# Performance work log

Measured on AMD Instinct MI355X. Metric: run time of the kernel, lower is better.

## Reference

```python
import jax, jax.numpy as jnp
import numpy as np

# ---- static configuration (matches init_kwargs / input_specs) ----
B, N = 4, 128            # images, proposals per image
C = 256                  # feature channels (in_channels)
HF, WF = 23, 30          # feature map size (input 736x960 / 32)
PH, PW = 7, 7            # pooled_size
SCALE = 1.0 / 32.0       # scale_factor
HIMG, WIMG = HF * 32, WF * 32
KH = HF // PH + 2        # max rows any pooling bin can span
KW = WF // PW + 2        # max cols any pooling bin can span
HID, OUT = 256, 5
NEG = -1e30


def _roi_pool_one(f, box):
    """Quantized ROI max pooling for one proposal.
    f: (C, HF, WF) feature map; box: (4,) [x1,y1,x2,y2] in feature coords.
    Returns (C, PH, PW)."""
    box = jax.lax.stop_gradient(box)  # indices are non-differentiable
    x1 = jnp.clip(jnp.floor(box[0]).astype(jnp.int32), 0, WF - 1)
    y1 = jnp.clip(jnp.floor(box[1]).astype(jnp.int32), 0, HF - 1)
    roi_w = jnp.clip(jnp.ceil(box[2]).astype(jnp.int32) - x1, 1, WF)
    roi_h = jnp.clip(jnp.ceil(box[3]).astype(jnp.int32) - y1, 1, HF)
    ph = jnp.arange(PH)
    pw = jnp.arange(PW)
    hs = y1 + (ph * roi_h) // PH                       # bin row starts (PH,)
    he = y1 + ((ph + 1) * roi_h + PH - 1) // PH        # bin row ends (ceil)
    ws = x1 + (pw * roi_w) // PW
    we = x1 + ((pw + 1) * roi_w + PW - 1) // PW
    hidx = hs[:, None] + jnp.arange(KH)[None, :]       # (PH, KH)
    hval = (hidx < he[:, None]) & (hidx < HF)
    widx = ws[:, None] + jnp.arange(KW)[None, :]       # (PW, KW)
    wval = (widx < we[:, None]) & (widx < WF)
    rows = f[:, jnp.clip(hidx, 0, HF - 1), :]          # (C, PH, KH, WF) gather
    rmax = jnp.max(jnp.where(hval[None, :, :, None], rows, NEG), axis=2)  # (C, PH, WF)
    cols = rmax[:, :, jnp.clip(widx, 0, WF - 1)]       # (C, PH, PW, KW) gather
    return jnp.max(jnp.where(wval[None, None], cols, NEG), axis=3)        # (C, PH, PW)


# vmap over proposals, then over images: (B,C,HF,WF),(B,N,4) -> (B,N,C,PH,PW)
_roi_pool = jax.vmap(jax.vmap(_roi_pool_one, in_axes=(None, 0)), in_axes=(0, 0))


def setup_inputs() -> dict:
    key = jax.random.key(0)
    ks = jax.random.split(key, 8)
    features = jax.random.normal(ks[0], (B, C, HF, WF), jnp.float32)
    # valid proposals in image coordinates (min box side ~32 px)
    x1 = jax.random.uniform(ks[1], (B, N)) * (WIMG - 32.0)
    y1 = jax.random.uniform(ks[2], (B, N)) * (HIMG - 32.0)
    x2 = x1 + 32.0 + jax.random.uniform(ks[3], (B, N)) * (WIMG - 32.0 - x1)
    y2 = y1 + 32.0 + jax.random.uniform(ks[4], (B, N)) * (HIMG - 32.0 - y1)
    conf = jax.random.normal(ks[5], (B, N))
    proposals = jnp.stack([x1, y1, x2, y2, conf], axis=-1)  # (B, N, 5)
    W1 = jax.random.normal(ks[6], (HID, C * PH * PW), jnp.float32) * 0.01
    b1 = jnp.zeros((HID,), jnp.float32)
    W2 = jax.random.normal(ks[7], (OUT, HID), jnp.float32) * 0.01
    b2 = jnp.zeros((OUT,), jnp.float32)
    return {"features": features, "proposals": proposals,
            "W1": W1, "b1": b1, "W2": W2, "b2": b2}


def reference(features, proposals, W1, b1, W2, b2):
    boxes_feat = proposals[..., :4] * SCALE                 # image -> feature coords
    pooled = _roi_pool(features, boxes_feat)                # (B, N, C, PH, PW)
    flat = pooled.reshape(B, N, C * PH * PW)
    h = jax.nn.relu(jnp.einsum('bnf,hf->bnh', flat, W1) + b1)
    out = jnp.einsum('bnh,oh->bno', h, W2) + b2             # (B, N, 5)
    refined_boxes = proposals[..., :4] + out[..., :4]
    refined_conf = jax.nn.sigmoid(proposals[..., 4:5] + out[..., 4:5])
    return jnp.concatenate([refined_boxes, refined_conf], axis=-1)  # (B, N, 5)
```

## Files before the change

### kernel.cpp

```cpp
#include <hip/hip_runtime.h>
#include <math.h>

#define Bq 4
#define Nq 128
#define Cq 256
#define HFq 23
#define WFq 30
#define PHq 7
#define PWq 7
#define HIDq 256
#define OUTq 5
#define Fq (Cq*PHq*PWq)
#define Mq (Bq*Nq)
#define HWq (HFq*WFq)
#define SCALEq (1.0f/32.0f)
#define NEGq (-1e30f)
#define KHq 5
#define KWq 6
#define SPLITK 14
#define KCH (Fq/SPLITK)
#define KSTEPS (KCH/32)

typedef float f32x4 __attribute__((ext_vector_type(4)));
typedef __bf16 bf16x8 __attribute__((ext_vector_type(8)));

__device__ __forceinline__ unsigned short f2b(float f) {
    unsigned int u = __float_as_uint(f);
    unsigned int r = (u + 0x7FFFu + ((u >> 16) & 1u)) >> 16;
    return (unsigned short)r;
}

__global__ __launch_bounds__(256) void k_transpose(const float* __restrict__ feat,
                                                   float* __restrict__ ft) {
    __shared__ float t[32][33];
    int bb = blockIdx.z;
    const float* src = feat + (size_t)bb * Cq * HWq;
    float* dst = ft + (size_t)bb * HWq * Cq;
    int x0 = blockIdx.x * 32;
    int c0 = blockIdx.y * 32;
    int tx = threadIdx.x, ty = threadIdx.y;
#pragma unroll
    for (int i = 0; i < 4; ++i) {
        int c = c0 + ty + i * 8;
        int x = x0 + tx;
        if (x < HWq) t[ty + i * 8][tx] = src[(size_t)c * HWq + x];
    }
    __syncthreads();
#pragma unroll
    for (int i = 0; i < 4; ++i) {
        int x = x0 + ty + i * 8;
        int c = c0 + tx;
        if (x < HWq) dst[(size_t)x * Cq + c] = t[tx][ty + i * 8];
    }
}

__global__ __launch_bounds__(256) void k_w1perm(const float* __restrict__ W1,
                                                unsigned short* __restrict__ w1p) {
    __shared__ __align__(16) unsigned short s[Fq];
    int j = blockIdx.x;
    const float4* src = (const float4*)(W1 + (size_t)j * Fq);
    for (int i = threadIdx.x; i < Fq / 4; i += 256) {
        float4 v = src[i];
        ushort4 o;
        o.x = f2b(v.x); o.y = f2b(v.y); o.z = f2b(v.z); o.w = f2b(v.w);
        ((ushort4*)s)[i] = o;
    }
    __syncthreads();
    uint4* dst = (uint4*)(w1p + (size_t)j * Fq);
    for (int i = threadIdx.x; i < Fq / 8; i += 256) {
        int base = i * 8;
        int cell = base >> 8;
        int c0 = base & 255;
        unsigned short tmp[8];
#pragma unroll
        for (int u = 0; u < 8; ++u) tmp[u] = s[(c0 + u) * 49 + cell];
        dst[i] = *(const uint4*)tmp;
    }
}

__global__ __launch_bounds__(256) void k_pool(const float* __restrict__ ft,
                                              const float* __restrict__ props,
                                              unsigned short* __restrict__ pooled) {
    int wave = threadIdx.x >> 6;
    int lane = threadIdx.x & 63;
    int g = blockIdx.y * 4 + wave;
    int m = blockIdx.x;
    int b = m >> 7;
    const float* pr = props + (size_t)m * 5;
    float b0 = pr[0] * SCALEq, b1v = pr[1] * SCALEq;
    float b2v = pr[2] * SCALEq, b3v = pr[3] * SCALEq;
    int x1 = min(max((int)floorf(b0), 0), WFq - 1);
    int y1 = min(max((int)floorf(b1v), 0), HFq - 1);
    int rw = min(max((int)ceilf(b2v) - x1, 1), WFq);
    int rh = min(max((int)ceilf(b3v) - y1, 1), HFq);
    const float* ftb = ft + (size_t)b * HWq * Cq + lane * 4;
    unsigned short* pm = pooled + (size_t)m * Fq + lane * 4;

    for (int cell = g; cell < PHq * PWq; cell += 8) {
        int ph = cell / 7;
        int pw = cell - ph * 7;
        int hs = y1 + (ph * rh) / PHq;
        int he = min(y1 + ((ph + 1) * rh + PHq - 1) / PHq, HFq);
        int ws = x1 + (pw * rw) / PWq;
        int we = min(x1 + ((pw + 1) * rw + PWq - 1) / PWq, WFq);
        f32x4 acc = {NEGq, NEGq, NEGq, NEGq};
#pragma unroll
        for (int kh = 0; kh < KHq; ++kh) {
            if (hs + kh < he) {
                const float* rowp = ftb + (size_t)((hs + kh) * WFq) * Cq;
#pragma unroll
                for (int kw = 0; kw < KWq; ++kw) {
                    if (ws + kw < we) {
                        f32x4 v = *(const f32x4*)(rowp + (size_t)(ws + kw) * Cq);
                        acc.x = fmaxf(acc.x, v.x);
                        acc.y = fmaxf(acc.y, v.y);
                        acc.z = fmaxf(acc.z, v.z);
                        acc.w = fmaxf(acc.w, v.w);
                    }
                }
            }
        }
        ushort4 o;
        o.x = f2b(acc.x); o.y = f2b(acc.y); o.z = f2b(acc.z); o.w = f2b(acc.w);
        *(ushort4*)(pm + (size_t)cell * Cq) = o;
    }
}

__global__ __launch_bounds__(256) void k_gemm1(const unsigned short* __restrict__ pooled,
                                               const unsigned short* __restrict__ w1p,
                                               float* __restrict__ part) {
    __shared__ __align__(16) unsigned short As[64 * 32];
    __shared__ __align__(16) unsigned short Bs[64 * 32];
    int m0 = blockIdx.x * 64;
    int j0 = blockIdx.y * 64;
    int kz = blockIdx.z;
    int tid = threadIdx.x;
    int r = tid >> 2, qq = tid & 3;
    const uint4* ap = (const uint4*)(pooled + (size_t)(m0 + r) * Fq + (size_t)kz * KCH + qq * 8);
    const uint4* bp = (const uint4*)(w1p + (size_t)(j0 + r) * Fq + (size_t)kz * KCH + qq * 8);
    int lane = tid & 63, wv = tid >> 6;
    int q = lane >> 4, mr = lane & 15;
    f32x4 acc0 = {0.f, 0.f, 0.f, 0.f};
    f32x4 acc1 = {0.f, 0.f, 0.f, 0.f};
    f32x4 acc2 = {0.f, 0.f, 0.f, 0.f};
    f32x4 acc3 = {0.f, 0.f, 0.f, 0.f};
    const bf16x8* afp = (const bf16x8*)(As + (wv * 16 + mr) * 32 + q * 8);
    const bf16x8* bfp0 = (const bf16x8*)(Bs + (0 + mr) * 32 + q * 8);
    const bf16x8* bfp1 = (const bf16x8*)(Bs + (16 + mr) * 32 + q * 8);
    const bf16x8* bfp2 = (const bf16x8*)(Bs + (32 + mr) * 32 + q * 8);
    const bf16x8* bfp3 = (const bf16x8*)(Bs + (48 + mr) * 32 + q * 8);
    uint4* asw = (uint4*)(As + r * 32 + qq * 8);
    uint4* bsw = (uint4*)(Bs + r * 32 + qq * 8);
    uint4 av = ap[0];
    uint4 bv = bp[0];
    for (int s = 0; s < KSTEPS; ++s) {
        __syncthreads();
        *asw = av;
        *bsw = bv;
        __syncthreads();
        if (s + 1 < KSTEPS) {
            av = ap[(s + 1) * 4];
            bv = bp[(s + 1) * 4];
        }
        bf16x8 a = *afp;
        acc0 = __builtin_amdgcn_mfma_f32_16x16x32_bf16(a, *bfp0, acc0, 0, 0, 0);
        acc1 = __builtin_amdgcn_mfma_f32_16x16x32_bf16(a, *bfp1, acc1, 0, 0, 0);
        acc2 = __builtin_amdgcn_mfma_f32_16x16x32_bf16(a, *bfp2, acc2, 0, 0, 0);
        acc3 = __builtin_amdgcn_mfma_f32_16x16x32_bf16(a, *bfp3, acc3, 0, 0, 0);
    }
    float* pbase = part + (size_t)kz * Mq * HIDq;
    int mb = m0 + wv * 16 + q * 4;
    int jj = j0 + mr;
#pragma unroll
    for (int r2 = 0; r2 < 4; ++r2) {
        float* row = pbase + (size_t)(mb + r2) * HIDq + jj;
        row[0]  = acc0[r2];
        row[16] = acc1[r2];
        row[32] = acc2[r2];
        row[48] = acc3[r2];
    }
}

__global__ __launch_bounds__(256) void k_reduce(const float* __restrict__ part,
                                                const float* __restrict__ b1,
                                                float* __restrict__ h) {
    int m = blockIdx.x, j = threadIdx.x;
    float s = 0.f;
#pragma unroll
    for (int z = 0; z < SPLITK; ++z) s += part[((size_t)z * Mq + m) * HIDq + j];
    s += b1[j];
    h[(size_t)m * HIDq + j] = fmaxf(s, 0.f);
}

__global__ __launch_bounds__(256) void k_final(const float* __restrict__ h,
                                               const float* __restrict__ W2,
                                               const float* __restrict__ b2,
                                               const float* __restrict__ props,
                                               float* __restrict__ out) {
    __shared__ float red[OUTq][4];
    int m = blockIdx.x, j = threadIdx.x;
    float hv = h[(size_t)m * HIDq + j];
    float p[OUTq];
#pragma unroll
    for (int o = 0; o < OUTq; ++o) p[o] = hv * W2[(size_t)o * HIDq + j];
    int lane = j & 63, wid = j >> 6;
#pragma unroll
    for (int o = 0; o < OUTq; ++o) {
        float v = p[o];
        v += __shfl_xor(v, 1);
        v += __shfl_xor(v, 2);
        v += __shfl_xor(v, 4);
        v += __shfl_xor(v, 8);
        v += __shfl_xor(v, 16);
        v += __shfl_xor(v, 32);
        if (lane == 0) red[o][wid] = v;
    }
    __syncthreads();
    if (j < OUTq) {
        float s = red[j][0] + red[j][1] + red[j][2] + red[j][3] + b2[j];
        float pv = props[(size_t)m * 5 + j];
        float r;
        if (j < 4) r = pv + s;
        else r = 1.f / (1.f + expf(-(pv + s)));
        out[(size_t)m * 5 + j] = r;
    }
}

extern "C" void kernel_launch(void* const* d_in, const int* in_sizes, int n_in,
                              void* d_out, int out_size, void* d_ws, size_t ws_size,
                              hipStream_t stream) {
    const float* feat  = (const float*)d_in[0];
    const float* props = (const float*)d_in[1];
    const float* W1    = (const float*)d_in[2];
    const float* b1    = (const float*)d_in[3];
    const float* W2    = (const float*)d_in[4];
    const float* b2    = (const float*)d_in[5];
    float* out = (float*)d_out;

    char* ws = (char*)d_ws;
    float* ft              = (float*)(ws);
    unsigned short* w1p    = (unsigned short*)(ws + 2826240);
    unsigned short* pooled = (unsigned short*)(ws + 9248768);
    float* part            = (float*)(ws + 22093824);
    float* h               = (float*)(ws + 29433856);

    k_transpose<<<dim3(22, 8, 4), dim3(32, 8), 0, stream>>>(feat, ft);
    k_w1perm<<<HIDq, 256, 0, stream>>>(W1, w1p);
    k_pool<<<dim3(Mq, 2), 256, 0, stream>>>(ft, props, pooled);
    k_gemm1<<<dim3(8, 4, SPLITK), 256, 0, stream>>>(pooled, w1p, part);
    k_reduce<<<Mq, 256, 0, stream>>>(part, b1, h);
    k_final<<<Mq, 256, 0, stream>>>(h, W2, b2, props, out);
}
```

Measured before the change: 128.7 us.

## Merge prep and tail kernels, store features as bf16, double-buffer GEMM LDS

After: 131.2 us. About the same (+2.0%).

```diff
diff --git a/kernel.cpp b/kernel.cpp
--- a/kernel.cpp
+++ b/kernel.cpp
@@ -17,9 +17,10 @@
 #define NEGq (-1e30f)
 #define KHq 5
 #define KWq 6
-#define SPLITK 14
+#define SPLITK 8
 #define KCH (Fq/SPLITK)
 #define KSTEPS (KCH/32)
+#define TJOBS 704
 
 typedef float f32x4 __attribute__((ext_vector_type(4)));
 typedef __bf16 bf16x8 __attribute__((ext_vector_type(8)));
@@ -29,56 +30,65 @@
     unsigned int r = (u + 0x7FFFu + ((u >> 16) & 1u)) >> 16;
     return (unsigned short)r;
 }
-
-__global__ __launch_bounds__(256) void k_transpose(const float* __restrict__ feat,
-                                                   float* __restrict__ ft) {
-    __shared__ float t[32][33];
-    int bb = blockIdx.z;
-    const float* src = feat + (size_t)bb * Cq * HWq;
-    float* dst = ft + (size_t)bb * HWq * Cq;
-    int x0 = blockIdx.x * 32;
-    int c0 = blockIdx.y * 32;
-    int tx = threadIdx.x, ty = threadIdx.y;
-#pragma unroll
-    for (int i = 0; i < 4; ++i) {
-        int c = c0 + ty + i * 8;
-        int x = x0 + tx;
-        if (x < HWq) t[ty + i * 8][tx] = src[(size_t)c * HWq + x];
-    }
-    __syncthreads();
-#pragma unroll
-    for (int i = 0; i < 4; ++i) {
-        int x = x0 + ty + i * 8;
-        int c = c0 + tx;
-        if (x < HWq) dst[(size_t)x * Cq + c] = t[tx][ty + i * 8];
-    }
-}
-
-__global__ __launch_bounds__(256) void k_w1perm(const float* __restrict__ W1,
-                                                unsigned short* __restrict__ w1p) {
-    __shared__ __align__(16) unsigned short s[Fq];
-    int j = blockIdx.x;
-    const float4* src = (const float4*)(W1 + (size_t)j * Fq);
-    for (int i = threadIdx.x; i < Fq / 4; i += 256) {
-        float4 v = src[i];
-        ushort4 o;
-        o.x = f2b(v.x); o.y = f2b(v.y); o.z = f2b(v.z); o.w = f2b(v.w);
-        ((ushort4*)s)[i] = o;
-    }
-    __syncthreads();
-    uint4* dst = (uint4*)(w1p + (size_t)j * Fq);
-    for (int i = threadIdx.x; i < Fq / 8; i += 256) {
-        int base = i * 8;
-        int cell = base >> 8;
-        int c0 = base & 255;
-        unsigned short tmp[8];
-#pragma unroll
-        for (int u = 0; u < 8; ++u) tmp[u] = s[(c0 + u) * 49 + cell];
-        dst[i] = *(const uint4*)tmp;
-    }
-}
-
-__global__ __launch_bounds__(256) void k_pool(const float* __restrict__ ft,
+__device__ __forceinline__ float b2f(unsigned short s) {
+    return __uint_as_float(((unsigned int)s) << 16);
+}
+
+union PrepSM {
+    float t[32][33];
+    unsigned short s[Fq];
+};
+
+__global__ __launch_bounds__(256) void k_prep(const float* __restrict__ feat,
+                                              const float* __restrict__ W1,
+                                              unsigned short* __restrict__ ft,
+                                              unsigned short* __restrict__ w1p) {
+    __shared__ __align__(16) PrepSM sm;
+    int tid = threadIdx.x, bid = blockIdx.x;
+    if (bid < TJOBS) {
+        int bb = bid / 176;
+        int rem = bid - bb * 176;
+        int cblk = rem / 22;
+        int xblk = rem - cblk * 22;
+        const float* src = feat + (size_t)bb * Cq * HWq;
+        unsigned short* dst = ft + (size_t)bb * HWq * Cq;
+        int x0 = xblk * 32, c0 = cblk * 32;
+        int tx = tid & 31, ty = tid >> 5;
+#pragma unroll
+        for (int i = 0; i < 4; ++i) {
+            int c = c0 + ty + i * 8, x = x0 + tx;
+            if (x < HWq) sm.t[ty + i * 8][tx] = src[(size_t)c * HWq + x];
+        }
+        __syncthreads();
+#pragma unroll
+        for (int i = 0; i < 4; ++i) {
+            int x = x0 + ty + i * 8, c = c0 + tx;
+            if (x < HWq) dst[(size_t)x * Cq + c] = f2b(sm.t[tx][ty + i * 8]);
+        }
+    } else {
+        int j = bid - TJOBS;
+        const float4* src = (const float4*)(W1 + (size_t)j * Fq);
+        for (int i = tid; i < Fq / 4; i += 256) {
+            float4 v = src[i];
+            ushort4 o;
+            o.x = f2b(v.x); o.y = f2b(v.y); o.z = f2b(v.z); o.w = f2b(v.w);
+            ((ushort4*)sm.s)[i] = o;
+        }
+        __syncthreads();
+        uint4* dst = (uint4*)(w1p + (size_t)j * Fq);
+        for (int i = tid; i < Fq / 8; i += 256) {
+            int base = i * 8;
+            int cell = base >> 8;
+            int c0 = base & 255;
+            unsigned short tmp[8];
+#pragma unroll
+            for (int u = 0; u < 8; ++u) tmp[u] = sm.s[(c0 + u) * 49 + cell];
+            dst[i] = *(const uint4*)tmp;
+        }
+    }
+}
+
+__global__ __launch_bounds__(256) void k_pool(const unsigned short* __restrict__ ft,
                                               const float* __restrict__ props,
                                               unsigned short* __restrict__ pooled) {
     int wave = threadIdx.x >> 6;
@@ -93,7 +103,7 @@
     int y1 = min(max((int)floorf(b1v), 0), HFq - 1);
     int rw = min(max((int)ceilf(b2v) - x1, 1), WFq);
     int rh = min(max((int)ceilf(b3v) - y1, 1), HFq);
-    const float* ftb = ft + (size_t)b * HWq * Cq + lane * 4;
+    const unsigned short* ftb = ft + (size_t)b * HWq * Cq + lane * 4;
     unsigned short* pm = pooled + (size_t)m * Fq + lane * 4;
 
     for (int cell = g; cell < PHq * PWq; cell += 8) {
@@ -101,21 +111,21 @@
         int pw = cell - ph * 7;
         int hs = y1 + (ph * rh) / PHq;
         int he = min(y1 + ((ph + 1) * rh + PHq - 1) / PHq, HFq);
-        int ws = x1 + (pw * rw) / PWq;
-        int we = min(x1 + ((pw + 1) * rw + PWq - 1) / PWq, WFq);
+        int wss = x1 + (pw * rw) / PWq;
+        int wee = min(x1 + ((pw + 1) * rw + PWq - 1) / PWq, WFq);
         f32x4 acc = {NEGq, NEGq, NEGq, NEGq};
 #pragma unroll
         for (int kh = 0; kh < KHq; ++kh) {
             if (hs + kh < he) {
-                const float* rowp = ftb + (size_t)((hs + kh) * WFq) * Cq;
+                const unsigned short* rowp = ftb + (size_t)((hs + kh) * WFq) * Cq;
 #pragma unroll
                 for (int kw = 0; kw < KWq; ++kw) {
-                    if (ws + kw < we) {
-                        f32x4 v = *(const f32x4*)(rowp + (size_t)(ws + kw) * Cq);
-                        acc.x = fmaxf(acc.x, v.x);
-                        acc.y = fmaxf(acc.y, v.y);
-                        acc.z = fmaxf(acc.z, v.z);
-                        acc.w = fmaxf(acc.w, v.w);
+                    if (wss + kw < wee) {
+                        ushort4 v = *(const ushort4*)(rowp + (size_t)(wss + kw) * Cq);
+                        acc.x = fmaxf(acc.x, b2f(v.x));
+                        acc.y = fmaxf(acc.y, b2f(v.y));
+                        acc.z = fmaxf(acc.z, b2f(v.z));
+                        acc.w = fmaxf(acc.w, b2f(v.w));
                     }
                 }
             }
@@ -129,8 +139,8 @@
 __global__ __launch_bounds__(256) void k_gemm1(const unsigned short* __restrict__ pooled,
                                                const unsigned short* __restrict__ w1p,
                                                float* __restrict__ part) {
-    __shared__ __align__(16) unsigned short As[64 * 32];
-    __shared__ __align__(16) unsigned short Bs[64 * 32];
+    __shared__ __align__(16) unsigned short As[2][2048];
+    __shared__ __align__(16) unsigned short Bs[2][2048];
     int m0 = blockIdx.x * 64;
     int j0 = blockIdx.y * 64;
     int kz = blockIdx.z;
@@ -144,29 +154,24 @@
     f32x4 acc1 = {0.f, 0.f, 0.f, 0.f};
     f32x4 acc2 = {0.f, 0.f, 0.f, 0.f};
     f32x4 acc3 = {0.f, 0.f, 0.f, 0.f};
-    const bf16x8* afp = (const bf16x8*)(As + (wv * 16 + mr) * 32 + q * 8);
-    const bf16x8* bfp0 = (const bf16x8*)(Bs + (0 + mr) * 32 + q * 8);
-    const bf16x8* bfp1 = (const bf16x8*)(Bs + (16 + mr) * 32 + q * 8);
-    const bf16x8* bfp2 = (const bf16x8*)(Bs + (32 + mr) * 32 + q * 8);
-    const bf16x8* bfp3 = (const bf16x8*)(Bs + (48 + mr) * 32 + q * 8);
-    uint4* asw = (uint4*)(As + r * 32 + qq * 8);
-    uint4* bsw = (uint4*)(Bs + r * 32 + qq * 8);
     uint4 av = ap[0];
     uint4 bv = bp[0];
     for (int s = 0; s < KSTEPS; ++s) {
-        __syncthreads();
-        *asw = av;
-        *bsw = bv;
+        int p = s & 1;
+        *(uint4*)(&As[p][tid * 8]) = av;
+        *(uint4*)(&Bs[p][tid * 8]) = bv;
         __syncthreads();
         if (s + 1 < KSTEPS) {
             av = ap[(s + 1) * 4];
             bv = bp[(s + 1) * 4];
         }
-        bf16x8 a = *afp;
-        acc0 = __builtin_amdgcn_mfma_f32_16x16x32_bf16(a, *bfp0, acc0, 0, 0, 0);
-        acc1 = __builtin_amdgcn_mfma_f32_16x16x32_bf16(a, *bfp1, acc1, 0, 0, 0);
-        acc2 = __builtin_amdgcn_mfma_f32_16x16x32_bf16(a, *bfp2, acc2, 0, 0, 0);
-        acc3 = __builtin_amdgcn_mfma_f32_16x16x32_bf16(a, *bfp3, acc3, 0, 0, 0);
+        const unsigned short* Ab = As[p];
+        const unsigned short* Bb = Bs[p];
+        bf16x8 a = *(const bf16x8*)(Ab + (wv * 16 + mr) * 32 + q * 8);
+        acc0 = __builtin_amdgcn_mfma_f32_16x16x32_bf16(a, *(const bf16x8*)(Bb + (0  + mr) * 32 + q * 8), acc0, 0, 0, 0);
+        acc1 = __builtin_amdgcn_mfma_f32_16x16x32_bf16(a, *(const bf16x8*)(Bb + (16 + mr) * 32 + q * 8), acc1, 0, 0, 0);
+        acc2 = __builtin_amdgcn_mfma_f32_16x16x32_bf16(a, *(const bf16x8*)(Bb + (32 + mr) * 32 + q * 8), acc2, 0, 0, 0);
+        acc3 = __builtin_amdgcn_mfma_f32_16x16x32_bf16(a, *(const bf16x8*)(Bb + (48 + mr) * 32 + q * 8), acc3, 0, 0, 0);
     }
     float* pbase = part + (size_t)kz * Mq * HIDq;
     int mb = m0 + wv * 16 + q * 4;
@@ -181,25 +186,19 @@
     }
 }
 
-__global__ __launch_bounds__(256) void k_reduce(const float* __restrict__ part,
-                                                const float* __restrict__ b1,
-                                                float* __restrict__ h) {
+__global__ __launch_bounds__(256) void k_tail(const float* __restrict__ part,
+                                              const float* __restrict__ b1,
+                                              const float* __restrict__ W2,
+                                              const float* __restrict__ b2,
+                                              const float* __restrict__ props,
+                                              float* __restrict__ out) {
+    __shared__ float red[OUTq][4];
     int m = blockIdx.x, j = threadIdx.x;
     float s = 0.f;
 #pragma unroll
     for (int z = 0; z < SPLITK; ++z) s += part[((size_t)z * Mq + m) * HIDq + j];
     s += b1[j];
-    h[(size_t)m * HIDq + j] = fmaxf(s, 0.f);
-}
-
-__global__ __launch_bounds__(256) void k_final(const float* __restrict__ h,
-                                               const float* __restrict__ W2,
-                                               const float* __restrict__ b2,
-                                               const float* __restrict__ props,
-                                               float* __restrict__ out) {
-    __shared__ float red[OUTq][4];
-    int m = blockIdx.x, j = threadIdx.x;
-    float hv = h[(size_t)m * HIDq + j];
+    float hv = fmaxf(s, 0.f);
     float p[OUTq];
 #pragma unroll
     for (int o = 0; o < OUTq; ++o) p[o] = hv * W2[(size_t)o * HIDq + j];
@@ -217,12 +216,12 @@
     }
     __syncthreads();
     if (j < OUTq) {
-        float s = red[j][0] + red[j][1] + red[j][2] + red[j][3] + b2[j];
+        float sv = red[j][0] + red[j][1] + red[j][2] + red[j][3] + b2[j];
         float pv = props[(size_t)m * 5 + j];
-        float r;
-        if (j < 4) r = pv + s;
-        else r = 1.f / (1.f + expf(-(pv + s)));
-        out[(size_t)m * 5 + j] = r;
+        float rr;
+        if (j < 4) rr = pv + sv;
+        else rr = 1.f / (1.f + expf(-(pv + sv)));
+        out[(size_t)m * 5 + j] = rr;
     }
 }
 
@@ -238,16 +237,13 @@
     float* out = (float*)d_out;
 
     char* ws = (char*)d_ws;
-    float* ft              = (float*)(ws);
-    unsigned short* w1p    = (unsigned short*)(ws + 2826240);
-    unsigned short* pooled = (unsigned short*)(ws + 9248768);
-    float* part            = (float*)(ws + 22093824);
-    float* h               = (float*)(ws + 29433856);
-
-    k_transpose<<<dim3(22, 8, 4), dim3(32, 8), 0, stream>>>(feat, ft);
-    k_w1perm<<<HIDq, 256, 0, stream>>>(W1, w1p);
+    unsigned short* ft     = (unsigned short*)(ws);
+    unsigned short* w1p    = (unsigned short*)(ws + 1413120);
+    unsigned short* pooled = (unsigned short*)(ws + 7835648);
+    float* part            = (float*)(ws + 20680704);
+
+    k_prep<<<TJOBS + HIDq, 256, 0, stream>>>(feat, W1, ft, w1p);
     k_pool<<<dim3(Mq, 2), 256, 0, stream>>>(ft, props, pooled);
     k_gemm1<<<dim3(8, 4, SPLITK), 256, 0, stream>>>(pooled, w1p, part);
-    k_reduce<<<Mq, 256, 0, stream>>>(part, b1, h);
-    k_final<<<Mq, 256, 0, stream>>>(h, W2, b2, props, out);
-}
+    k_tail<<<Mq, 256, 0, stream>>>(part, b1, W2, b2, props, out);
+}
```
